# Optimization experiments

Hardware: AMD Instinct MI355X
Metric: run time of the kernel (lower is better)

Reference implementation:

```python
import jax, jax.numpy as jnp
import numpy as np

B, C, H, W = 4, 96, 64, 64
CS = 8                      # chunk size
DN = 2 * C                  # d_inner (expand=2)
N = 16                      # d_state
K = 4                       # scan directions
DT_R = (C + 15) // 16       # dt_rank = ceil(d_model/16)
EPS = 1e-5


def _ln(x, g, b):
    m = x.mean(-1, keepdims=True)
    v = ((x - m) ** 2).mean(-1, keepdims=True)
    return (x - m) / jnp.sqrt(v + EPS) * g + b


def _selective_scan(xs, delta, A, Bs, Cs, D):
    # xs, delta: (Bc, K, Dn, L); Bs, Cs: (Bc, K, N, L); A: (K, Dn, N); D: (K, Dn)
    Bc, Kk, Dn, L = xs.shape
    uT = xs.transpose(3, 0, 1, 2)       # (L, Bc, K, Dn)
    dT = delta.transpose(3, 0, 1, 2)
    BT = Bs.transpose(3, 0, 1, 2)       # (L, Bc, K, N)
    CT = Cs.transpose(3, 0, 1, 2)

    def step(h, inp):
        u_l, d_l, B_l, C_l = inp
        dA = jnp.exp(d_l[..., None] * A)                       # (Bc,K,Dn,N)
        h = h * dA + (d_l * u_l)[..., None] * B_l[:, :, None, :]
        y = jnp.einsum('bkdn,bkn->bkd', h, C_l)
        return h, y

    h0 = jnp.zeros((Bc, Kk, Dn, A.shape[-1]), xs.dtype)
    _, ys = jax.lax.scan(step, h0, (uT, dT, BT, CT))           # ys: (L,Bc,K,Dn)
    ys = ys.transpose(1, 2, 3, 0)                              # (Bc,K,Dn,L)
    return ys + D[None, :, :, None] * xs


def _ss2d(xh, in_proj_w, conv_w, conv_b, x_proj_w, dt_w, dt_b,
          A_logs, Ds, outnorm_g, outnorm_b, out_proj_w):
    # xh: (Bc, Hc, Wc, C)
    Bc, Hc, Wc, _ = xh.shape
    L = Hc * Wc
    xz = xh @ in_proj_w                                        # (Bc,Hc,Wc,2*Dn)
    xc, z = jnp.split(xz, 2, axis=-1)
    xc = xc.transpose(0, 3, 1, 2)                              # (Bc,Dn,Hc,Wc)
    xc = jax.lax.conv_general_dilated(xc, conv_w, (1, 1), ((1, 1), (1, 1)),
                                      feature_group_count=DN)
    xc = jax.nn.silu(xc + conv_b[None, :, None, None])
    x0 = xc.reshape(Bc, DN, L)                                 # HW order
    x1 = xc.transpose(0, 1, 3, 2).reshape(Bc, DN, L)           # WH order
    xs = jnp.stack([x0, x1, x0[:, :, ::-1], x1[:, :, ::-1]], axis=1)  # (Bc,4,Dn,L)
    x_dbl = jnp.einsum('bkdl,kcd->bkcl', xs, x_proj_w)         # (Bc,4,DT_R+2N,L)
    dts = x_dbl[:, :, :DT_R]
    Bs = x_dbl[:, :, DT_R:DT_R + N]
    Cs = x_dbl[:, :, DT_R + N:]
    dts = jnp.einsum('bkrl,kdr->bkdl', dts, dt_w)
    delta = jax.nn.softplus(dts + dt_b[None, :, :, None])      # (Bc,4,Dn,L)
    A = -jnp.exp(A_logs).reshape(K, DN, N)
    ys = _selective_scan(xs, delta, A, Bs, Cs, Ds.reshape(K, DN))
    y0 = ys[:, 0]
    y1 = ys[:, 1].reshape(Bc, DN, Wc, Hc).transpose(0, 1, 3, 2).reshape(Bc, DN, L)
    y2 = ys[:, 2, :, ::-1]
    y3 = ys[:, 3, :, ::-1].reshape(Bc, DN, Wc, Hc).transpose(0, 1, 3, 2).reshape(Bc, DN, L)
    y = (y0 + y1 + y2 + y3).transpose(0, 2, 1)                 # (Bc,L,Dn)
    y = _ln(y, outnorm_g, outnorm_b).reshape(Bc, Hc, Wc, DN)
    y = y * jax.nn.silu(z)
    return y @ out_proj_w                                      # (Bc,Hc,Wc,C)


def reference(x, gamma, beta, alpha, ln1_g, ln1_b, in_proj_w, conv_w, conv_b,
              x_proj_w, dt_w, dt_b, A_logs, Ds, outnorm_g, outnorm_b, out_proj_w):
    Bb, Cc, Hh, Ww = x.shape
    # StateNorm: per (b, c) over spatial dims, unbiased=False
    mean = x.mean(axis=(2, 3), keepdims=True)
    var = ((x - mean) ** 2).mean(axis=(2, 3), keepdims=True)
    x_norm = (x - mean) / jnp.sqrt(var + EPS)
    x_norm = gamma[None, :, None, None] * x_norm + beta[None, :, None, None]
    x_act = jax.nn.silu(x_norm)                 # act_quant with bits=32 is identity
    hn, wn = Hh // CS, Ww // CS
    # chunk: b c (hn cs)(wn cs) -> (b hn wn) c cs cs
    xc = x_act.reshape(Bb, Cc, hn, CS, wn, CS).transpose(0, 2, 4, 1, 3, 5)
    xc = xc.reshape(Bb * hn * wn, Cc, CS, CS)
    # VSSBlock: h + SS2D(LN(h)) in BHWC (drop_path = identity at inference)
    h = xc.transpose(0, 2, 3, 1)                # (Bc, cs, cs, C)
    h = h + _ss2d(_ln(h, ln1_g, ln1_b), in_proj_w, conv_w, conv_b, x_proj_w,
                  dt_w, dt_b, A_logs, Ds, outnorm_g, outnorm_b, out_proj_w)
    xv = h.transpose(0, 3, 1, 2)                # back to BCHW
    # unchunk
    xv = xv.reshape(Bb, hn, wn, Cc, CS, CS).transpose(0, 3, 1, 4, 2, 5)
    xv = xv.reshape(Bb, Cc, Hh, Ww)
    return x + alpha * xv


def setup_inputs() -> dict:
    key = jax.random.key(0)
    ks = jax.random.split(key, 12)
    s = 0.02
    inp = {
        'x': jax.random.normal(ks[0], (B, C, H, W), jnp.float32),
        'gamma': jnp.ones((C,), jnp.float32),
        'beta': jnp.zeros((C,), jnp.float32),
        'alpha': jnp.float32(0.5),
        'ln1_g': jnp.ones((C,), jnp.float32),
        'ln1_b': jnp.zeros((C,), jnp.float32),
        'in_proj_w': jax.random.normal(ks[1], (C, 2 * DN), jnp.float32) / np.sqrt(C),
        'conv_w': jax.random.normal(ks[2], (DN, 1, 3, 3), jnp.float32) / 3.0,
        'conv_b': jnp.zeros((DN,), jnp.float32),
        'x_proj_w': jax.random.normal(ks[3], (K, DT_R + 2 * N, DN), jnp.float32) / np.sqrt(DN),
        'dt_w': jax.random.normal(ks[4], (K, DN, DT_R), jnp.float32) * (DT_R ** -0.5),
        'dt_b': jnp.full((K, DN), -4.6, jnp.float32) + s * jax.random.normal(ks[5], (K, DN), jnp.float32),
        'A_logs': jnp.log(jnp.broadcast_to(jnp.arange(1, N + 1, dtype=jnp.float32), (K * DN, N))).copy(),
        'Ds': jnp.ones((K * DN,), jnp.float32),
        'outnorm_g': jnp.ones((DN,), jnp.float32),
        'outnorm_b': jnp.zeros((DN,), jnp.float32),
        'out_proj_w': jax.random.normal(ks[6], (DN, C), jnp.float32) / np.sqrt(DN),
    }
    return inp
```

## Files before the change

kernel.cpp:

```cpp
#include <hip/hip_runtime.h>
#include <math.h>

__device__ __forceinline__ float siluf_(float x) {
    return x / (1.f + __expf(-x));
}

__device__ __forceinline__ int sperm(int k, int l) {
    int t = (k & 1) ? (((l & 7) << 3) | (l >> 3)) : l;
    return (k & 2) ? (63 - t) : t;
}

__device__ __forceinline__ unsigned int f2bf(float f) {
    unsigned int u = __float_as_uint(f);
    return (u + 0x7FFFu + ((u >> 16) & 1u)) >> 16;
}
__device__ __forceinline__ float bf2f(unsigned int h) {
    return __uint_as_float(h << 16);
}
__device__ __forceinline__ unsigned int packbf(float lo, float hi) {
    return f2bf(lo) | (f2bf(hi) << 16);
}

__global__ void k1a_stats(const float* __restrict__ x, float* __restrict__ stats) {
    int bc = blockIdx.x;
    const float* xp = x + (size_t)bc * 4096;
    float s = 0.f, sq = 0.f;
    for (int i = threadIdx.x; i < 4096; i += 256) {
        float v = xp[i]; s += v; sq += v * v;
    }
    __shared__ float rs[256], rq[256];
    rs[threadIdx.x] = s; rq[threadIdx.x] = sq;
    __syncthreads();
    for (int off = 128; off > 0; off >>= 1) {
        if (threadIdx.x < off) {
            rs[threadIdx.x] += rs[threadIdx.x + off];
            rq[threadIdx.x] += rq[threadIdx.x + off];
        }
        __syncthreads();
    }
    if (threadIdx.x == 0) {
        float m = rs[0] * (1.f / 4096.f);
        float v = rq[0] * (1.f / 4096.f) - m * m;
        stats[bc] = m;
        stats[384 + bc] = rsqrtf(v + 1e-5f);
    }
}

__global__ __launch_bounds__(256) void kA(
        const float* __restrict__ x, const float* __restrict__ stats,
        const float* __restrict__ gamma, const float* __restrict__ beta,
        const float* __restrict__ ln1_g, const float* __restrict__ ln1_b,
        const float* __restrict__ Win,
        float* __restrict__ xcg_all,
        unsigned int* __restrict__ zg_b) {
    int blk = blockIdx.x;
    int xcd = blk & 7, j = blk >> 3;
    int chunk = xcd * 32 + (j >> 2), cg = j & 3;
    int b = chunk >> 6, chh = (chunk >> 3) & 7, chw = chunk & 7;
    __shared__ float hs[64 * 97];
    int t = threadIdx.x;
    for (int i = t; i < 6144; i += 256) {
        int c = i >> 6, pos = i & 63;
        int bc = b * 96 + c;
        int hh = chh * 8 + (pos >> 3), ww = chw * 8 + (pos & 7);
        float v = x[(((size_t)bc) * 64 + hh) * 64 + ww];
        float xn = (v - stats[bc]) * stats[384 + bc] * gamma[c] + beta[c];
        hs[pos * 97 + c] = siluf_(xn);
    }
    __syncthreads();
    {
        int p = t >> 2, o = t & 3;
        float s = 0.f, sq = 0.f;
        #pragma unroll
        for (int jj = 0; jj < 24; jj++) { float v = hs[p * 97 + o + 4 * jj]; s += v; sq += v * v; }
        s += __shfl_xor(s, 1); sq += __shfl_xor(sq, 1);
        s += __shfl_xor(s, 2); sq += __shfl_xor(sq, 2);
        float m = s * (1.f / 96.f);
        float rinv = rsqrtf(sq * (1.f / 96.f) - m * m + 1e-5f);
        #pragma unroll
        for (int jj = 0; jj < 24; jj++) {
            int c = o + 4 * jj;
            hs[p * 97 + c] = (hs[p * 97 + c] - m) * rinv * ln1_g[c] + ln1_b[c];
        }
    }
    __syncthreads();
    int p = t & 63;
    int wv = __builtin_amdgcn_readfirstlane(t >> 6);
    int jbase = cg * 96 + wv * 24;
    float acc[24];
    #pragma unroll
    for (int i = 0; i < 24; i++) acc[i] = 0.f;
    for (int c = 0; c < 96; c++) {
        float u = hs[p * 97 + c];
        const float* w = Win + c * 384 + jbase;
        #pragma unroll
        for (int i = 0; i < 24; i++) acc[i] = fmaf(u, w[i], acc[i]);
    }
    if (jbase < 192) {
        float* o_ = xcg_all + (size_t)chunk * 12288 + jbase * 64 + p;
        #pragma unroll
        for (int i = 0; i < 24; i++) o_[i * 64] = acc[i];
    } else {
        int i2base = (jbase - 192) >> 1;
        unsigned int* o_ = zg_b + (size_t)chunk * 6144 + i2base * 64 + p;
        #pragma unroll
        for (int i = 0; i < 12; i++) o_[i * 64] = packbf(acc[2 * i], acc[2 * i + 1]);
    }
}

__global__ __launch_bounds__(256) void kB(
        const float* __restrict__ xcg_all, const float* __restrict__ conv_w,
        const float* __restrict__ conv_b, float* __restrict__ x0T_all) {
    int blk = blockIdx.x;
    int xcd = blk & 7, j = blk >> 3;
    int chunk = xcd * 32 + (j >> 2), dg = j & 3;
    int dbase = dg * 48;
    __shared__ float tile[48 * 65];
    int t = threadIdx.x;
    const float* in = xcg_all + (size_t)chunk * 12288 + dbase * 64;
    for (int i = t; i < 3072; i += 256) tile[(i >> 6) * 65 + (i & 63)] = in[i];
    __syncthreads();
    float* o = x0T_all + (size_t)chunk * 12288;
    for (int s = 0; s < 12; s++) {
        int idx = s * 256 + t;
        int l = idx / 48, dl = idx - l * 48;
        int r = l >> 3, cc = l & 7;
        int d = dbase + dl;
        float acc = conv_b[d];
        #pragma unroll
        for (int dh = 0; dh < 3; dh++) {
            int rr = r + dh - 1;
            if (rr < 0 || rr > 7) continue;
            #pragma unroll
            for (int dw = 0; dw < 3; dw++) {
                int cw = cc + dw - 1;
                if (cw < 0 || cw > 7) continue;
                acc = fmaf(tile[dl * 65 + rr * 8 + cw], conv_w[d * 9 + dh * 3 + dw], acc);
            }
        }
        o[l * 192 + d] = siluf_(acc);
    }
}

__global__ __launch_bounds__(192) void kD(
        const float* __restrict__ x0T_all, const float* __restrict__ xpw,
        const float* __restrict__ dtw, const float* __restrict__ dtb,
        const float* __restrict__ A_logs, const float* __restrict__ Ds,
        float* __restrict__ yac_all) {
    int blk = blockIdx.x;
    int xcd = blk & 7, j = blk >> 3;
    int chunk = xcd * 32 + (j >> 2);
    int k = j & 3;
    __shared__ float pT[64 * 40];
    int t = threadIdx.x;
    const float* xbase = x0T_all + (size_t)chunk * 12288;

    {
        int l = t & 63;
        int wv3 = __builtin_amdgcn_readfirstlane(t >> 6);
        int cbase = wv3 * 13;
        float acc[13];
        #pragma unroll
        for (int i = 0; i < 13; i++) acc[i] = 0.f;
        const float* xl = xbase + l * 192;
        const float* wb = xpw + (size_t)k * 38 * 192;
        for (int dd = 0; dd < 192; dd += 4) {
            float4 u4 = *(const float4*)(xl + dd);
            #pragma unroll
            for (int ci = 0; ci < 13; ci++) {
                int c = cbase + ci;
                if (c < 38) {
                    float4 w4 = *(const float4*)(wb + c * 192 + dd);
                    acc[ci] = fmaf(u4.x, w4.x, acc[ci]);
                    acc[ci] = fmaf(u4.y, w4.y, acc[ci]);
                    acc[ci] = fmaf(u4.z, w4.z, acc[ci]);
                    acc[ci] = fmaf(u4.w, w4.w, acc[ci]);
                }
            }
        }
        #pragma unroll
        for (int ci = 0; ci < 13; ci++) {
            int c = cbase + ci;
            if (c < 38) {
                int slot = c + (c >= 6 ? 2 : 0);
                pT[l * 40 + slot] = acc[ci];
            }
        }
    }
    __syncthreads();

    {
        int d = t;
        int gd = k * 192 + d;
        float w6[6];
        #pragma unroll
        for (int r = 0; r < 6; r++) w6[r] = dtw[gd * 6 + r];
        float bias = dtb[gd];
        float Dd = Ds[gd];
        float a[16];
        #pragma unroll
        for (int n = 0; n < 16; n++) a[n] = -__expf(A_logs[gd * 16 + n]);
        bool pw = true;
        #pragma unroll
        for (int n = 1; n < 16; n++)
            pw = pw && (fabsf(a[n] - (float)(n + 1) * a[0]) <= 1e-4f * fabsf(a[n]) + 1e-6f);
        float hst[16];
        #pragma unroll
        for (int n = 0; n < 16; n++) hst[n] = 0.f;
        float* yo = yac_all + (size_t)chunk * 12288;

        if (__all(pw)) {
            float a0 = a[0];
            float u_nxt = xbase[sperm(k, 0) * 192 + d];
            for (int l = 0; l < 64; l++) {
                int sl = sperm(k, l);
                const float4* r4 = (const float4*)(pT + sl * 40);
                float4 rA = r4[0], rB = r4[1];
                float4 b0 = r4[2], b1 = r4[3], b2 = r4[4], b3 = r4[5];
                float4 c0 = r4[6], c1 = r4[7], c2 = r4[8], c3 = r4[9];
                float u = u_nxt;
                if (l < 63) u_nxt = xbase[sperm(k, l + 1) * 192 + d];
                float dp = bias;
                dp = fmaf(rA.x, w6[0], dp); dp = fmaf(rA.y, w6[1], dp);
                dp = fmaf(rA.z, w6[2], dp); dp = fmaf(rA.w, w6[3], dp);
                dp = fmaf(rB.x, w6[4], dp); dp = fmaf(rB.y, w6[5], dp);
                float delta = (dp > 20.f) ? dp : __logf(1.f + __expf(dp));
                float du = delta * u;
                float e1 = __expf(delta * a0);
                float p[16];
                p[0] = e1;
                p[1] = e1 * e1;
                p[2] = p[1] * e1;   p[3] = p[1] * p[1];
                p[4] = p[3] * e1;   p[5] = p[3] * p[1];
                p[6] = p[3] * p[2]; p[7] = p[3] * p[3];
                p[8] = p[7] * e1;   p[9] = p[7] * p[1];
                p[10] = p[7] * p[2]; p[11] = p[7] * p[3];
                p[12] = p[7] * p[4]; p[13] = p[7] * p[5];
                p[14] = p[7] * p[6]; p[15] = p[7] * p[7];
                float y0 = 0.f, y1 = 0.f, y2 = 0.f, y3 = 0.f;
                hst[0]  = fmaf(hst[0],  p[0],  du * b0.x); y0 = fmaf(hst[0],  c0.x, y0);
                hst[1]  = fmaf(hst[1],  p[1],  du * b0.y); y1 = fmaf(hst[1],  c0.y, y1);
                hst[2]  = fmaf(hst[2],  p[2],  du * b0.z); y2 = fmaf(hst[2],  c0.z, y2);
                hst[3]  = fmaf(hst[3],  p[3],  du * b0.w); y3 = fmaf(hst[3],  c0.w, y3);
                hst[4]  = fmaf(hst[4],  p[4],  du * b1.x); y0 = fmaf(hst[4],  c1.x, y0);
                hst[5]  = fmaf(hst[5],  p[5],  du * b1.y); y1 = fmaf(hst[5],  c1.y, y1);
                hst[6]  = fmaf(hst[6],  p[6],  du * b1.z); y2 = fmaf(hst[6],  c1.z, y2);
                hst[7]  = fmaf(hst[7],  p[7],  du * b1.w); y3 = fmaf(hst[7],  c1.w, y3);
                hst[8]  = fmaf(hst[8],  p[8],  du * b2.x); y0 = fmaf(hst[8],  c2.x, y0);
                hst[9]  = fmaf(hst[9],  p[9],  du * b2.y); y1 = fmaf(hst[9],  c2.y, y1);
                hst[10] = fmaf(hst[10], p[10], du * b2.z); y2 = fmaf(hst[10], c2.z, y2);
                hst[11] = fmaf(hst[11], p[11], du * b2.w); y3 = fmaf(hst[11], c2.w, y3);
                hst[12] = fmaf(hst[12], p[12], du * b3.x); y0 = fmaf(hst[12], c3.x, y0);
                hst[13] = fmaf(hst[13], p[13], du * b3.y); y1 = fmaf(hst[13], c3.y, y1);
                hst[14] = fmaf(hst[14], p[14], du * b3.z); y2 = fmaf(hst[14], c3.z, y2);
                hst[15] = fmaf(hst[15], p[15], du * b3.w); y3 = fmaf(hst[15], c3.w, y3);
                atomicAdd(&yo[sl * 192 + d], (y0 + y1) + (y2 + y3) + Dd * u);
            }
        } else {
            for (int l = 0; l < 64; l++) {
                int sl = sperm(k, l);
                float u = xbase[sl * 192 + d];
                const float* row = pT + sl * 40;
                float dp = bias;
                #pragma unroll
                for (int r = 0; r < 6; r++) dp = fmaf(row[r + (r >= 6 ? 2 : 0)], w6[r], dp);
                float delta = (dp > 20.f) ? dp : __logf(1.f + __expf(dp));
                float du = delta * u;
                float y = 0.f;
                #pragma unroll
                for (int n = 0; n < 16; n++) {
                    float e = __expf(delta * a[n]);
                    hst[n] = fmaf(hst[n], e, du * row[8 + n]);
                    y = fmaf(hst[n], row[24 + n], y);
                }
                atomicAdd(&yo[sl * 192 + d], y + Dd * u);
            }
        }
    }
}

__global__ __launch_bounds__(256) void kE(
        const float* __restrict__ yac_all, const unsigned int* __restrict__ zg_b,
        const float* __restrict__ og, const float* __restrict__ ob,
        float* __restrict__ g_all) {
    int blk = blockIdx.x;
    int xcd = blk & 7, j = blk >> 3;
    int chunk = xcd * 32 + (j >> 1), half = j & 1;
    int t = threadIdx.x;
    int p = half * 32 + (t >> 3), o = t & 7;
    int par = o & 1;
    const float* yrow = yac_all + (size_t)chunk * 12288 + p * 192;
    float ys[24];
    float s = 0.f, sq = 0.f;
    #pragma unroll
    for (int jj = 0; jj < 24; jj++) {
        float v = yrow[o + 8 * jj];
        ys[jj] = v; s += v; sq += v * v;
    }
    s += __shfl_xor(s, 1); sq += __shfl_xor(sq, 1);
    s += __shfl_xor(s, 2); sq += __shfl_xor(sq, 2);
    s += __shfl_xor(s, 4); sq += __shfl_xor(sq, 4);
    float m = s * (1.f / 192.f);
    float rinv = rsqrtf(sq * (1.f / 192.f) - m * m + 1e-5f);
    const unsigned int* z = zg_b + (size_t)chunk * 6144;
    float* g = g_all + (size_t)chunk * 12288;
    #pragma unroll
    for (int jj = 0; jj < 24; jj++) {
        int i = o + 8 * jj;
        float ln = (ys[jj] - m) * rinv * og[i] + ob[i];
        unsigned int zw = z[(i >> 1) * 64 + p];
        float zv = bf2f(par ? (zw >> 16) : (zw & 0xFFFFu));
        g[i * 64 + p] = ln * siluf_(zv);
    }
}

__global__ __launch_bounds__(256) void kF(
        const float* __restrict__ g_all, const float* __restrict__ Wout,
        const float* __restrict__ x, const float* __restrict__ stats,
        const float* __restrict__ gamma, const float* __restrict__ beta,
        const float* __restrict__ alpha, float* __restrict__ out) {
    int blk = blockIdx.x;
    int xcd = blk & 7, j = blk >> 3;
    int chunk = xcd * 32 + (j >> 2), cgf = j & 3;
    int b = chunk >> 6, chh = (chunk >> 3) & 7, chw = chunk & 7;
    int t = threadIdx.x;
    int p = t & 63;
    int wv = __builtin_amdgcn_readfirstlane(t >> 6);
    int cbase = cgf * 24 + wv * 6;
    float acc[6];
    #pragma unroll
    for (int i = 0; i < 6; i++) acc[i] = 0.f;
    const float* g = g_all + (size_t)chunk * 12288;
    for (int dd = 0; dd < 192; dd++) {
        float u = g[dd * 64 + p];
        const float* w = Wout + dd * 96 + cbase;
        #pragma unroll
        for (int i = 0; i < 6; i++) acc[i] = fmaf(u, w[i], acc[i]);
    }
    float al = alpha[0];
    int hh = chh * 8 + (p >> 3), ww = chw * 8 + (p & 7);
    #pragma unroll
    for (int i = 0; i < 6; i++) {
        int c = cbase + i;
        int bc = b * 96 + c;
        size_t gi = (((size_t)bc) * 64 + hh) * 64 + ww;
        float xv = x[gi];
        float xn = (xv - stats[bc]) * stats[384 + bc] * gamma[c] + beta[c];
        out[gi] = xv + al * (siluf_(xn) + acc[i]);
    }
}

extern "C" void kernel_launch(void* const* d_in, const int* in_sizes, int n_in,
                              void* d_out, int out_size, void* d_ws, size_t ws_size,
                              hipStream_t stream) {
    const float* x        = (const float*)d_in[0];
    const float* gamma    = (const float*)d_in[1];
    const float* beta     = (const float*)d_in[2];
    const float* alpha    = (const float*)d_in[3];
    const float* ln1_g    = (const float*)d_in[4];
    const float* ln1_b    = (const float*)d_in[5];
    const float* in_proj  = (const float*)d_in[6];
    const float* conv_w   = (const float*)d_in[7];
    const float* conv_b   = (const float*)d_in[8];
    const float* x_proj   = (const float*)d_in[9];
    const float* dt_w     = (const float*)d_in[10];
    const float* dt_b     = (const float*)d_in[11];
    const float* A_logs   = (const float*)d_in[12];
    const float* Ds       = (const float*)d_in[13];
    const float* onorm_g  = (const float*)d_in[14];
    const float* onorm_b  = (const float*)d_in[15];
    const float* out_proj = (const float*)d_in[16];
    float* out = (float*)d_out;

    float* ws    = (float*)d_ws;
    float* stats = ws;
    float* xcg   = ws + 768;
    float* x0T   = xcg + 3145728;
    unsigned int* zg_b = (unsigned int*)(x0T + 3145728);
    float* yac   = xcg;
    float* gbuf  = x0T;

    hipLaunchKernelGGL(k1a_stats, dim3(384), dim3(256), 0, stream, x, stats);
    hipLaunchKernelGGL(kA, dim3(1024), dim3(256), 0, stream,
                       x, stats, gamma, beta, ln1_g, ln1_b, in_proj, xcg, zg_b);
    hipLaunchKernelGGL(kB, dim3(1024), dim3(256), 0, stream,
                       xcg, conv_w, conv_b, x0T);
    hipMemsetAsync(yac, 0, (size_t)3145728 * 4, stream);
    hipLaunchKernelGGL(kD, dim3(1024), dim3(192), 0, stream,
                       x0T, x_proj, dt_w, dt_b, A_logs, Ds, yac);
    hipLaunchKernelGGL(kE, dim3(512), dim3(256), 0, stream,
                       yac, zg_b, onorm_g, onorm_b, gbuf);
    hipLaunchKernelGGL(kF, dim3(1024), dim3(256), 0, stream,
                       gbuf, out_proj, x, stats, gamma, beta, alpha, out);
}
```

Measured before the change: 208.0 us.

## Replace atomic y accumulation with per-direction bf16 buffers summed in norm kernel

The scan kernel no longer atomically adds fp32 outputs of the four directions into one zeroed buffer. Each direction now writes its own packed-bf16 output plane, with adjacent channel pairs packed via a lane shuffle. The LayerNorm/gate kernel reads and sums the four planes. This removes the memset and the atomic traffic. The scan loop also software-prefetches the next step's shared-memory row, adds an occupancy hint to launch bounds, and cleans up the fallback indexing. The cost is bf16 rounding of each partial sum, extra reads in the norm kernel, and higher register pressure from the prefetch.

```diff
diff --git a/kernel.cpp b/kernel.cpp
--- a/kernel.cpp
+++ b/kernel.cpp
@@ -142,11 +142,12 @@
     }
 }
 
-__global__ __launch_bounds__(192) void kD(
+__global__ __launch_bounds__(192, 3) void kD(
         const float* __restrict__ x0T_all, const float* __restrict__ xpw,
         const float* __restrict__ dtw, const float* __restrict__ dtb,
         const float* __restrict__ A_logs, const float* __restrict__ Ds,
-        float* __restrict__ yac_all) {
+        unsigned int* __restrict__ yk01,
+        unsigned int* __restrict__ yk23) {
     int blk = blockIdx.x;
     int xcd = blk & 7, j = blk >> 3;
     int chunk = xcd * 32 + (j >> 2);
@@ -207,19 +208,25 @@
         float hst[16];
         #pragma unroll
         for (int n = 0; n < 16; n++) hst[n] = 0.f;
-        float* yo = yac_all + (size_t)chunk * 12288;
+        unsigned int* yb = (k < 2 ? yk01 : yk23) + (size_t)(k & 1) * 1572864
+                           + (size_t)chunk * 6144;
 
         if (__all(pw)) {
             float a0 = a[0];
-            float u_nxt = xbase[sperm(k, 0) * 192 + d];
+            int sl = sperm(k, 0);
+            const float4* r4 = (const float4*)(pT + sl * 40);
+            float4 rA = r4[0], rB = r4[1];
+            float4 b0 = r4[2], b1 = r4[3], b2 = r4[4], b3 = r4[5];
+            float4 c0 = r4[6], c1 = r4[7], c2 = r4[8], c3 = r4[9];
+            float u = xbase[sl * 192 + d];
+            #pragma unroll 2
             for (int l = 0; l < 64; l++) {
-                int sl = sperm(k, l);
-                const float4* r4 = (const float4*)(pT + sl * 40);
-                float4 rA = r4[0], rB = r4[1];
-                float4 b0 = r4[2], b1 = r4[3], b2 = r4[4], b3 = r4[5];
-                float4 c0 = r4[6], c1 = r4[7], c2 = r4[8], c3 = r4[9];
-                float u = u_nxt;
-                if (l < 63) u_nxt = xbase[sperm(k, l + 1) * 192 + d];
+                int sl_n = sperm(k, (l + 1) & 63);
+                const float4* n4 = (const float4*)(pT + sl_n * 40);
+                float4 nA = n4[0], nB = n4[1];
+                float4 nb0 = n4[2], nb1 = n4[3], nb2 = n4[4], nb3 = n4[5];
+                float4 nc0 = n4[6], nc1 = n4[7], nc2 = n4[8], nc3 = n4[9];
+                float u_n = xbase[sl_n * 192 + d];
                 float dp = bias;
                 dp = fmaf(rA.x, w6[0], dp); dp = fmaf(rA.y, w6[1], dp);
                 dp = fmaf(rA.z, w6[2], dp); dp = fmaf(rA.w, w6[3], dp);
@@ -254,7 +261,14 @@
                 hst[13] = fmaf(hst[13], p[13], du * b3.y); y1 = fmaf(hst[13], c3.y, y1);
                 hst[14] = fmaf(hst[14], p[14], du * b3.z); y2 = fmaf(hst[14], c3.z, y2);
                 hst[15] = fmaf(hst[15], p[15], du * b3.w); y3 = fmaf(hst[15], c3.w, y3);
-                atomicAdd(&yo[sl * 192 + d], (y0 + y1) + (y2 + y3) + Dd * u);
+                float yv = (y0 + y1) + (y2 + y3) + Dd * u;
+                float yo = __shfl_xor(yv, 1);
+                unsigned int wpack = packbf(yv, yo);
+                if ((d & 1) == 0) yb[sl * 96 + (d >> 1)] = wpack;
+                rA = nA; rB = nB;
+                b0 = nb0; b1 = nb1; b2 = nb2; b3 = nb3;
+                c0 = nc0; c1 = nc1; c2 = nc2; c3 = nc3;
+                u = u_n; sl = sl_n;
             }
         } else {
             for (int l = 0; l < 64; l++) {
@@ -263,7 +277,7 @@
                 const float* row = pT + sl * 40;
                 float dp = bias;
                 #pragma unroll
-                for (int r = 0; r < 6; r++) dp = fmaf(row[r + (r >= 6 ? 2 : 0)], w6[r], dp);
+                for (int r = 0; r < 6; r++) dp = fmaf(row[r], w6[r], dp);
                 float delta = (dp > 20.f) ? dp : __logf(1.f + __expf(dp));
                 float du = delta * u;
                 float y = 0.f;
@@ -273,14 +287,18 @@
                     hst[n] = fmaf(hst[n], e, du * row[8 + n]);
                     y = fmaf(hst[n], row[24 + n], y);
                 }
-                atomicAdd(&yo[sl * 192 + d], y + Dd * u);
+                float yv = y + Dd * u;
+                float yo = __shfl_xor(yv, 1);
+                unsigned int wpack = packbf(yv, yo);
+                if ((d & 1) == 0) yb[sl * 96 + (d >> 1)] = wpack;
             }
         }
     }
 }
 
 __global__ __launch_bounds__(256) void kE(
-        const float* __restrict__ yac_all, const unsigned int* __restrict__ zg_b,
+        const unsigned int* __restrict__ yk01, const unsigned int* __restrict__ yk23,
+        const unsigned int* __restrict__ zg_b,
         const float* __restrict__ og, const float* __restrict__ ob,
         float* __restrict__ g_all) {
     int blk = blockIdx.x;
@@ -289,12 +307,20 @@
     int t = threadIdx.x;
     int p = half * 32 + (t >> 3), o = t & 7;
     int par = o & 1;
-    const float* yrow = yac_all + (size_t)chunk * 12288 + p * 192;
+    size_t rb = (size_t)chunk * 6144 + p * 96;
+    const unsigned int* r0 = yk01 + rb;
+    const unsigned int* r1 = yk01 + 1572864 + rb;
+    const unsigned int* r2 = yk23 + rb;
+    const unsigned int* r3 = yk23 + 1572864 + rb;
     float ys[24];
     float s = 0.f, sq = 0.f;
     #pragma unroll
     for (int jj = 0; jj < 24; jj++) {
-        float v = yrow[o + 8 * jj];
+        int i = o + 8 * jj;
+        int wi = i >> 1;
+        int sh = par ? 16 : 0;
+        float v = bf2f((r0[wi] >> sh) & 0xFFFFu) + bf2f((r1[wi] >> sh) & 0xFFFFu)
+                + bf2f((r2[wi] >> sh) & 0xFFFFu) + bf2f((r3[wi] >> sh) & 0xFFFFu);
         ys[jj] = v; s += v; sq += v * v;
     }
     s += __shfl_xor(s, 1); sq += __shfl_xor(sq, 1);
@@ -377,7 +403,8 @@
     float* xcg   = ws + 768;
     float* x0T   = xcg + 3145728;
     unsigned int* zg_b = (unsigned int*)(x0T + 3145728);
-    float* yac   = xcg;
+    unsigned int* yk23 = zg_b + 1572864;
+    unsigned int* yk01 = (unsigned int*)xcg;
     float* gbuf  = x0T;
 
     hipLaunchKernelGGL(k1a_stats, dim3(384), dim3(256), 0, stream, x, stats);
@@ -385,11 +412,10 @@
                        x, stats, gamma, beta, ln1_g, ln1_b, in_proj, xcg, zg_b);
     hipLaunchKernelGGL(kB, dim3(1024), dim3(256), 0, stream,
                        xcg, conv_w, conv_b, x0T);
-    hipMemsetAsync(yac, 0, (size_t)3145728 * 4, stream);
     hipLaunchKernelGGL(kD, dim3(1024), dim3(192), 0, stream,
-                       x0T, x_proj, dt_w, dt_b, A_logs, Ds, yac);
+                       x0T, x_proj, dt_w, dt_b, A_logs, Ds, yk01, yk23);
     hipLaunchKernelGGL(kE, dim3(512), dim3(256), 0, stream,
-                       yac, zg_b, onorm_g, onorm_b, gbuf);
+                       yk01, yk23, zg_b, onorm_g, onorm_b, gbuf);
     hipLaunchKernelGGL(kF, dim3(1024), dim3(256), 0, stream,
                        gbuf, out_proj, x, stats, gamma, beta, alpha, out);
 }
```

Measured after the change: 208.6 us. Within noise of the previous version (+0.3%).
